# Kernel tuning notes

Hardware: AMD Instinct MI355X
Metric: run time of the kernel (lower is better)

The kernel has to match this reference:

```python
import jax, jax.numpy as jnp
import numpy as np

DISTANCES = [1, 2]
ANGLES_DEG = [0.0, 45.0, 90.0, 135.0]
LEVELS = 32
FEATURES = ["contrast", "homogeneity", "energy", "correlation"]

# skimage graycomatrix offsets: row = r + round(sin(a)*d), col = c + round(cos(a)*d)
OFFSETS = [(int(np.round(np.sin(np.deg2rad(a)) * d)), int(np.round(np.cos(np.deg2rad(a)) * d)))
           for d in DISTANCES for a in ANGLES_DEG]


def _quantize(images, levels):
    # RGB -> gray, [-1,1] -> [0,1] -> integer gray levels (uint8 floor cast in original)
    gray = images.mean(axis=1)                                  # [B,H,W]
    g = jnp.clip((gray + 1.0) * 0.5 * (levels - 1), 0.0, levels - 1)
    return g.astype(jnp.int32)


def _glcm(g, dr, dc, levels):
    # symmetric, normed co-occurrence matrix for one (distance, angle) offset
    B, H, W = g.shape
    r0, r1 = max(0, -dr), H - max(0, dr)
    c0, c1 = max(0, -dc), W - max(0, dc)
    i = g[:, r0:r1, c0:c1]
    j = g[:, r0 + dr:r1 + dr, c0 + dc:c1 + dc]
    idx = (i * levels + j).reshape(B, -1)                        # [B, n_pairs]
    hist = jax.vmap(lambda ix: jnp.zeros(levels * levels, jnp.float32).at[ix].add(1.0))(idx)
    P = hist.reshape(B, levels, levels)
    P = P + jnp.swapaxes(P, 1, 2)                                # symmetric
    return P / jnp.sum(P, axis=(1, 2), keepdims=True)            # normed


def _prop(P, feat):
    # graycoprops formulas; P: [B, L, L]
    L = P.shape[-1]
    I = jnp.arange(L, dtype=jnp.float32)[:, None]                # [L,1]
    J = jnp.arange(L, dtype=jnp.float32)[None, :]                # [1,L]
    if feat == "contrast":
        return jnp.sum(P * (I - J) ** 2, axis=(1, 2))
    if feat == "homogeneity":
        return jnp.sum(P / (1.0 + (I - J) ** 2), axis=(1, 2))
    if feat == "energy":
        return jnp.sqrt(jnp.sum(P * P, axis=(1, 2)))
    if feat == "correlation":
        mu_i = jnp.sum(I * P, axis=(1, 2))                       # [B]
        mu_j = jnp.sum(J * P, axis=(1, 2))
        di = I[None] - mu_i[:, None, None]
        dj = J[None] - mu_j[:, None, None]
        std_i = jnp.sqrt(jnp.sum(P * di * di, axis=(1, 2)))
        std_j = jnp.sqrt(jnp.sum(P * dj * dj, axis=(1, 2)))
        cov = jnp.sum(P * di * dj, axis=(1, 2))
        denom = std_i * std_j
        return jnp.where(denom > 1e-15, cov / jnp.where(denom > 1e-15, denom, 1.0), 1.0)
    raise ValueError(feat)


def reference(images):
    g = _quantize(images, LEVELS)
    # accumulate feature values over all (distance, angle) offsets, then mean
    acc = {f: 0.0 for f in FEATURES}
    for (dr, dc) in OFFSETS:
        P = _glcm(g, dr, dc, LEVELS)
        for f in FEATURES:
            acc[f] = acc[f] + _prop(P, f)
    n = float(len(OFFSETS))
    return jnp.stack([acc[f] / n for f in FEATURES], axis=0)     # [n_features, B]


def setup_inputs() -> dict:
    key = jax.random.key(0)
    images = jax.random.normal(key, (64, 3, 512, 512), dtype=jnp.float32)
    return {"images": images}
```

## Files before the change

kernel.cpp:

```cpp
#include <hip/hip_runtime.h>

#define NIMG 64
#define NUQ 6
#define NSTRIP 16
#define SROWS 32
#define HW (512 * 512)

__device__ __constant__ float UOFF_W[NUQ] = {1.f, 2.f, 1.f, 2.f, 1.f, 1.f};
#define DR_PACK 0x201110u
#define DCP_PACK 0x130122u

__device__ __forceinline__ unsigned char quant1(float x, float y, float z) {
    float gray = (x + y + z) / 3.0f;
    float t = (gray + 1.0f) * 0.5f * 31.0f;
    t = fminf(fmaxf(t, 0.0f), 31.0f);
    return (unsigned char)(int)t;
}

__device__ __forceinline__ void ppair(int i, int j, unsigned int* __restrict__ hu) {
    int d = (i << 4) | ((i + (j >> 1)) & 15);
    atomicAdd(&hu[d], 1u << ((j & 1) << 4));
}

__global__ __launch_bounds__(256) void glcm_fused(
    const float* __restrict__ in, unsigned int* __restrict__ hist_g) {
    const int b = blockIdx.x >> 4;
    const int s = blockIdx.x & 15;
    const int rs = s * SROWS;

    __shared__ unsigned char ring[4 * 2048];
    __shared__ unsigned int hist[NUQ * 512];

    const int tid = threadIdx.x;
    for (int k = tid; k < NUQ * 512; k += 256) hist[k] = 0;

    const float* ib = in + (size_t)b * (3 * HW);
    const int lrow = tid >> 6;
    const int lcol = (tid & 63) << 3;

    float4 A0, B0, A1, B1, A2, B2;

    for (int c = 0; c <= 9; ++c) {
        const int gr = rs + (c << 2) + lrow;
        const bool doload = (c <= 8) && ((c << 2) + lrow < SROWS + 2) && (gr < 512);
        if (doload) {
            const float* p = ib + ((size_t)gr << 9) + lcol;
            A0 = *(const float4*)(p);
            B0 = *(const float4*)(p + 4);
            A1 = *(const float4*)(p + HW);
            B1 = *(const float4*)(p + HW + 4);
            A2 = *(const float4*)(p + 2 * HW);
            B2 = *(const float4*)(p + 2 * HW + 4);
        }

        if (c >= 2) {
            const int k = c - 2;
            for (int idx = tid; idx < 768; idx += 256) {
                int u = idx >> 7;
                int rem = idx & 127;
                int r4 = rem >> 5;
                int g = rem & 31;
                int dr = (DR_PACK >> (u << 2)) & 15;
                int dc = (int)((DCP_PACK >> (u << 2)) & 15) - 1;
                int R = (k << 2) + r4;
                int nr_u = min(512 - dr - rs, SROWS);
                int gA = (dc < 0) ? 1 : 0;
                int gEnd = (dc > 0) ? 31 : 32;
                if (R < nr_u && g >= gA && g < gEnd) {
                    const uint4* ip = (const uint4*)(ring + ((k & 3) << 11) + (r4 << 9) + (g << 4));
                    uint4 iw = *ip;
                    int Rj = R + dr;
                    int jbase = (((Rj >> 2) & 3) << 11) + ((Rj & 3) << 9);
                    unsigned int jw0, jw1, jw2, jw3;
                    if (dc == 0) {
                        uint4 jv = *(const uint4*)(ring + jbase + (g << 4));
                        jw0 = jv.x; jw1 = jv.y; jw2 = jv.z; jw3 = jv.w;
                    } else {
                        int jb = jbase + (g << 4) + dc;
                        const unsigned int* t32 = (const unsigned int*)(ring + (jb & ~3));
                        int sb = (jb & 3) << 3;
                        unsigned int w0 = t32[0], w1 = t32[1], w2 = t32[2],
                                     w3 = t32[3], w4 = t32[4];
                        jw0 = (w0 >> sb) | (w1 << (32 - sb));
                        jw1 = (w1 >> sb) | (w2 << (32 - sb));
                        jw2 = (w2 >> sb) | (w3 << (32 - sb));
                        jw3 = (w3 >> sb) | (w4 << (32 - sb));
                    }
                    unsigned int* hu = hist + (u << 9);
                    #pragma unroll
                    for (int q = 0; q < 4; ++q) {
                        ppair((iw.x >> (8 * q)) & 255, (jw0 >> (8 * q)) & 255, hu);
                        ppair((iw.y >> (8 * q)) & 255, (jw1 >> (8 * q)) & 255, hu);
                        ppair((iw.z >> (8 * q)) & 255, (jw2 >> (8 * q)) & 255, hu);
                        ppair((iw.w >> (8 * q)) & 255, (jw3 >> (8 * q)) & 255, hu);
                    }
                }
            }
            for (int idx = tid; idx < 384; idx += 256) {
                int u = idx >> 6;
                int rem = idx & 63;
                int r4 = rem >> 4;
                int e = rem & 15;
                int dr = (DR_PACK >> (u << 2)) & 15;
                int dc = (int)((DCP_PACK >> (u << 2)) & 15) - 1;
                int elen = (dc == 0) ? 0 : ((dc == 2) ? 14 : 15);
                int ebase = (dc < 0) ? 1 : 496;
                int R = (k << 2) + r4;
                int nr_u = min(512 - dr - rs, SROWS);
                if (e < elen && R < nr_u) {
                    int ci = ebase + e;
                    int ia = ((k & 3) << 11) + (r4 << 9) + ci;
                    int Rj = R + dr;
                    int ja = (((Rj >> 2) & 3) << 11) + ((Rj & 3) << 9) + ci + dc;
                    ppair(ring[ia], ring[ja], hist + (u << 9));
                }
            }
        }

        if (doload) {
            unsigned int q0 =
                (unsigned int)quant1(A0.x, A1.x, A2.x)
                | ((unsigned int)quant1(A0.y, A1.y, A2.y) << 8)
                | ((unsigned int)quant1(A0.z, A1.z, A2.z) << 16)
                | ((unsigned int)quant1(A0.w, A1.w, A2.w) << 24);
            unsigned int q1 =
                (unsigned int)quant1(B0.x, B1.x, B2.x)
                | ((unsigned int)quant1(B0.y, B1.y, B2.y) << 8)
                | ((unsigned int)quant1(B0.z, B1.z, B2.z) << 16)
                | ((unsigned int)quant1(B0.w, B1.w, B2.w) << 24);
            uint2* wp = (uint2*)(ring + ((c & 3) << 11) + (lrow << 9) + lcol);
            *wp = make_uint2(q0, q1);
        }
        __syncthreads();
    }

    unsigned int* hb = hist_g + (size_t)blockIdx.x * (NUQ * 512);
    for (int k = tid; k < NUQ * 512; k += 256) hb[k] = hist[k];
}

__global__ __launch_bounds__(256) void feature_kernel(
    const unsigned int* __restrict__ hist_g, float* __restrict__ feats) {
    const int blk = blockIdx.x;
    const int b = blk / NUQ;
    const int u = blk - b * NUQ;
    const int dr = (DR_PACK >> (u << 2)) & 15;
    const int dc = (int)((DCP_PACK >> (u << 2)) & 15) - 1;
    const int adc = dc < 0 ? -dc : dc;
    const float inv_total = 1.0f / (2.0f * (float)((512 - dr) * (512 - adc)));

    __shared__ unsigned int cnt[1024];
    __shared__ float red[4][6];
    const int tid = threadIdx.x;
    const int wid = tid >> 6;
    const int lane = tid & 63;

    for (int d = tid; d < 512; d += 256) {
        unsigned int lo = 0, hi = 0;
        const unsigned int* p = hist_g + ((size_t)(b * NSTRIP) * NUQ + u) * 512 + d;
        #pragma unroll
        for (int st = 0; st < NSTRIP; ++st) {
            unsigned int v = p[(size_t)st * NUQ * 512];
            lo += v & 0xffffu;
            hi += v >> 16;
        }
        int i = d >> 4;
        int jh = ((d & 15) - i) & 15;
        cnt[(i << 5) | (jh << 1)] = lo;
        cnt[(i << 5) | (jh << 1) | 1] = hi;
    }
    __syncthreads();

    float c_sum = 0.f, h_sum = 0.f, e_sum = 0.f, m1 = 0.f, m2 = 0.f, m12 = 0.f;
    for (int k = tid; k < 1024; k += 256) {
        int i = k >> 5, j = k & 31;
        float sym = (float)(cnt[k] + cnt[(j << 5) | i]);
        float P = sym * inv_total;
        float d = (float)(i - j);
        float d2 = d * d;
        float fi = (float)i, fj = (float)j;
        c_sum += P * d2;
        h_sum += P / (1.0f + d2);
        e_sum += P * P;
        m1  += P * fi;
        m2  += P * fi * fi;
        m12 += P * fi * fj;
    }
    #pragma unroll
    for (int sft = 32; sft > 0; sft >>= 1) {
        c_sum += __shfl_down(c_sum, sft);
        h_sum += __shfl_down(h_sum, sft);
        e_sum += __shfl_down(e_sum, sft);
        m1    += __shfl_down(m1, sft);
        m2    += __shfl_down(m2, sft);
        m12   += __shfl_down(m12, sft);
    }
    if (lane == 0) {
        red[wid][0] = c_sum; red[wid][1] = h_sum; red[wid][2] = e_sum;
        red[wid][3] = m1;    red[wid][4] = m2;    red[wid][5] = m12;
    }
    __syncthreads();
    if (tid == 0) {
        float rc = 0, rh = 0, re2 = 0, rm1 = 0, rm2 = 0, rm12 = 0;
        #pragma unroll
        for (int w = 0; w < 4; ++w) {
            rc += red[w][0]; rh += red[w][1]; re2 += red[w][2];
            rm1 += red[w][3]; rm2 += red[w][4]; rm12 += red[w][5];
        }
        float mu  = rm1;
        float var = rm2 - mu * mu;
        float cov = rm12 - mu * mu;
        float denom = var;
        float corr = (denom > 1e-15f) ? cov / denom : 1.0f;
        float* f = feats + (size_t)blk * 4;
        f[0] = rc;
        f[1] = rh;
        f[2] = sqrtf(re2);
        f[3] = corr;
    }
}

__global__ __launch_bounds__(256) void reduce_kernel(
    const float* __restrict__ feats, float* __restrict__ out) {
    int tid = threadIdx.x;
    int f = tid >> 6, b = tid & 63;
    float s = 0.f;
    #pragma unroll
    for (int u = 0; u < NUQ; ++u) s += UOFF_W[u] * feats[(size_t)(b * NUQ + u) * 4 + f];
    out[f * NIMG + b] = s * 0.125f;
}

extern "C" void kernel_launch(void* const* d_in, const int* in_sizes, int n_in,
                              void* d_out, int out_size, void* d_ws, size_t ws_size,
                              hipStream_t stream) {
    const float* images = (const float*)d_in[0];
    float* out = (float*)d_out;

    unsigned int* hist_g = (unsigned int*)d_ws;
    size_t hbytes = (size_t)NIMG * NSTRIP * NUQ * 512 * sizeof(unsigned int);
    float* feats = (float*)((char*)d_ws + hbytes);

    glcm_fused<<<NIMG * NSTRIP, 256, 0, stream>>>(images, hist_g);
    feature_kernel<<<NIMG * NUQ, 256, 0, stream>>>(hist_g, feats);
    reduce_kernel<<<1, 256, 0, stream>>>(feats, out);
}
```

Measured before the change: 65.28 us.

## Double-buffer global loads in GLCM kernel and fuse feature and reduce kernels

The main histogram kernel now keeps two register sets for loaded tiles, so each tile's global loads are issued one stage before it is quantized. This gives the loads a full histogram stage to complete before their data is used. Separately, the per-offset feature kernel and the final reduce kernel are merged into one kernel per image, which drops a launch and the intermediate feature buffer. The costs are higher register pressure from the duplicated float4 buffers and fewer blocks (64) in the feature stage.

```diff
diff --git a/kernel.cpp b/kernel.cpp
--- a/kernel.cpp
+++ b/kernel.cpp
@@ -38,12 +38,10 @@
     const int lrow = tid >> 6;
     const int lcol = (tid & 63) << 3;
 
-    float4 A0, B0, A1, B1, A2, B2;
-
-    for (int c = 0; c <= 9; ++c) {
+    auto issueL = [&](int c, float4& A0, float4& B0, float4& A1, float4& B1,
+                      float4& A2, float4& B2) {
         const int gr = rs + (c << 2) + lrow;
-        const bool doload = (c <= 8) && ((c << 2) + lrow < SROWS + 2) && (gr < 512);
-        if (doload) {
+        if ((c << 2) + lrow < SROWS + 2 && gr < 512) {
             const float* p = ib + ((size_t)gr << 9) + lcol;
             A0 = *(const float4*)(p);
             B0 = *(const float4*)(p + 4);
@@ -52,72 +50,12 @@
             A2 = *(const float4*)(p + 2 * HW);
             B2 = *(const float4*)(p + 2 * HW + 4);
         }
-
-        if (c >= 2) {
-            const int k = c - 2;
-            for (int idx = tid; idx < 768; idx += 256) {
-                int u = idx >> 7;
-                int rem = idx & 127;
-                int r4 = rem >> 5;
-                int g = rem & 31;
-                int dr = (DR_PACK >> (u << 2)) & 15;
-                int dc = (int)((DCP_PACK >> (u << 2)) & 15) - 1;
-                int R = (k << 2) + r4;
-                int nr_u = min(512 - dr - rs, SROWS);
-                int gA = (dc < 0) ? 1 : 0;
-                int gEnd = (dc > 0) ? 31 : 32;
-                if (R < nr_u && g >= gA && g < gEnd) {
-                    const uint4* ip = (const uint4*)(ring + ((k & 3) << 11) + (r4 << 9) + (g << 4));
-                    uint4 iw = *ip;
-                    int Rj = R + dr;
-                    int jbase = (((Rj >> 2) & 3) << 11) + ((Rj & 3) << 9);
-                    unsigned int jw0, jw1, jw2, jw3;
-                    if (dc == 0) {
-                        uint4 jv = *(const uint4*)(ring + jbase + (g << 4));
-                        jw0 = jv.x; jw1 = jv.y; jw2 = jv.z; jw3 = jv.w;
-                    } else {
-                        int jb = jbase + (g << 4) + dc;
-                        const unsigned int* t32 = (const unsigned int*)(ring + (jb & ~3));
-                        int sb = (jb & 3) << 3;
-                        unsigned int w0 = t32[0], w1 = t32[1], w2 = t32[2],
-                                     w3 = t32[3], w4 = t32[4];
-                        jw0 = (w0 >> sb) | (w1 << (32 - sb));
-                        jw1 = (w1 >> sb) | (w2 << (32 - sb));
-                        jw2 = (w2 >> sb) | (w3 << (32 - sb));
-                        jw3 = (w3 >> sb) | (w4 << (32 - sb));
-                    }
-                    unsigned int* hu = hist + (u << 9);
-                    #pragma unroll
-                    for (int q = 0; q < 4; ++q) {
-                        ppair((iw.x >> (8 * q)) & 255, (jw0 >> (8 * q)) & 255, hu);
-                        ppair((iw.y >> (8 * q)) & 255, (jw1 >> (8 * q)) & 255, hu);
-                        ppair((iw.z >> (8 * q)) & 255, (jw2 >> (8 * q)) & 255, hu);
-                        ppair((iw.w >> (8 * q)) & 255, (jw3 >> (8 * q)) & 255, hu);
-                    }
-                }
-            }
-            for (int idx = tid; idx < 384; idx += 256) {
-                int u = idx >> 6;
-                int rem = idx & 63;
-                int r4 = rem >> 4;
-                int e = rem & 15;
-                int dr = (DR_PACK >> (u << 2)) & 15;
-                int dc = (int)((DCP_PACK >> (u << 2)) & 15) - 1;
-                int elen = (dc == 0) ? 0 : ((dc == 2) ? 14 : 15);
-                int ebase = (dc < 0) ? 1 : 496;
-                int R = (k << 2) + r4;
-                int nr_u = min(512 - dr - rs, SROWS);
-                if (e < elen && R < nr_u) {
-                    int ci = ebase + e;
-                    int ia = ((k & 3) << 11) + (r4 << 9) + ci;
-                    int Rj = R + dr;
-                    int ja = (((Rj >> 2) & 3) << 11) + ((Rj & 3) << 9) + ci + dc;
-                    ppair(ring[ia], ring[ja], hist + (u << 9));
-                }
-            }
-        }
-
-        if (doload) {
+    };
+
+    auto quantW = [&](int c, const float4& A0, const float4& B0, const float4& A1,
+                      const float4& B1, const float4& A2, const float4& B2) {
+        const int gr = rs + (c << 2) + lrow;
+        if ((c << 2) + lrow < SROWS + 2 && gr < 512) {
             unsigned int q0 =
                 (unsigned int)quant1(A0.x, A1.x, A2.x)
                 | ((unsigned int)quant1(A0.y, A1.y, A2.y) << 8)
@@ -131,102 +69,172 @@
             uint2* wp = (uint2*)(ring + ((c & 3) << 11) + (lrow << 9) + lcol);
             *wp = make_uint2(q0, q1);
         }
-        __syncthreads();
+    };
+
+    auto histF = [&](int k) {
+        for (int idx = tid; idx < 768; idx += 256) {
+            int u = idx >> 7;
+            int rem = idx & 127;
+            int r4 = rem >> 5;
+            int g = rem & 31;
+            int dr = (DR_PACK >> (u << 2)) & 15;
+            int dc = (int)((DCP_PACK >> (u << 2)) & 15) - 1;
+            int R = (k << 2) + r4;
+            int nr_u = min(512 - dr - rs, SROWS);
+            int gA = (dc < 0) ? 1 : 0;
+            int gEnd = (dc > 0) ? 31 : 32;
+            if (R < nr_u && g >= gA && g < gEnd) {
+                const uint4* ip = (const uint4*)(ring + ((k & 3) << 11) + (r4 << 9) + (g << 4));
+                uint4 iw = *ip;
+                int Rj = R + dr;
+                int jbase = (((Rj >> 2) & 3) << 11) + ((Rj & 3) << 9);
+                unsigned int jw0, jw1, jw2, jw3;
+                if (dc == 0) {
+                    uint4 jv = *(const uint4*)(ring + jbase + (g << 4));
+                    jw0 = jv.x; jw1 = jv.y; jw2 = jv.z; jw3 = jv.w;
+                } else {
+                    int jb = jbase + (g << 4) + dc;
+                    const unsigned int* t32 = (const unsigned int*)(ring + (jb & ~3));
+                    int sb = (jb & 3) << 3;
+                    unsigned int w0 = t32[0], w1 = t32[1], w2 = t32[2],
+                                 w3 = t32[3], w4 = t32[4];
+                    jw0 = (w0 >> sb) | (w1 << (32 - sb));
+                    jw1 = (w1 >> sb) | (w2 << (32 - sb));
+                    jw2 = (w2 >> sb) | (w3 << (32 - sb));
+                    jw3 = (w3 >> sb) | (w4 << (32 - sb));
+                }
+                unsigned int* hu = hist + (u << 9);
+                #pragma unroll
+                for (int q = 0; q < 4; ++q) {
+                    ppair((iw.x >> (8 * q)) & 255, (jw0 >> (8 * q)) & 255, hu);
+                    ppair((iw.y >> (8 * q)) & 255, (jw1 >> (8 * q)) & 255, hu);
+                    ppair((iw.z >> (8 * q)) & 255, (jw2 >> (8 * q)) & 255, hu);
+                    ppair((iw.w >> (8 * q)) & 255, (jw3 >> (8 * q)) & 255, hu);
+                }
+            }
+        }
+        for (int idx = tid; idx < 384; idx += 256) {
+            int u = idx >> 6;
+            int rem = idx & 63;
+            int r4 = rem >> 4;
+            int e = rem & 15;
+            int dr = (DR_PACK >> (u << 2)) & 15;
+            int dc = (int)((DCP_PACK >> (u << 2)) & 15) - 1;
+            int elen = (dc == 0) ? 0 : ((dc == 2) ? 14 : 15);
+            int ebase = (dc < 0) ? 1 : 496;
+            int R = (k << 2) + r4;
+            int nr_u = min(512 - dr - rs, SROWS);
+            if (e < elen && R < nr_u) {
+                int ci = ebase + e;
+                int ia = ((k & 3) << 11) + (r4 << 9) + ci;
+                int Rj = R + dr;
+                int ja = (((Rj >> 2) & 3) << 11) + ((Rj & 3) << 9) + ci + dc;
+                ppair(ring[ia], ring[ja], hist + (u << 9));
+            }
+        }
+    };
+
+    float4 zA0 = {0,0,0,0}, zB0 = {0,0,0,0}, zA1 = {0,0,0,0},
+           zB1 = {0,0,0,0}, zA2 = {0,0,0,0}, zB2 = {0,0,0,0};
+    float4 yA0 = {0,0,0,0}, yB0 = {0,0,0,0}, yA1 = {0,0,0,0},
+           yB1 = {0,0,0,0}, yA2 = {0,0,0,0}, yB2 = {0,0,0,0};
+
+    for (int cc = 0; cc < 12; cc += 2) {
+        {
+            const int c = cc;
+            if (c <= 8) issueL(c, zA0, zB0, zA1, zB1, zA2, zB2);
+            if (c >= 3 && c <= 10) histF(c - 3);
+            if (c >= 1 && c <= 9) quantW(c - 1, yA0, yB0, yA1, yB1, yA2, yB2);
+            __syncthreads();
+        }
+        {
+            const int c = cc + 1;
+            if (c <= 8) issueL(c, yA0, yB0, yA1, yB1, yA2, yB2);
+            if (c >= 3 && c <= 10) histF(c - 3);
+            if (c >= 1 && c <= 9) quantW(c - 1, zA0, zB0, zA1, zB1, zA2, zB2);
+            __syncthreads();
+        }
     }
 
     unsigned int* hb = hist_g + (size_t)blockIdx.x * (NUQ * 512);
     for (int k = tid; k < NUQ * 512; k += 256) hb[k] = hist[k];
 }
 
-__global__ __launch_bounds__(256) void feature_kernel(
-    const unsigned int* __restrict__ hist_g, float* __restrict__ feats) {
-    const int blk = blockIdx.x;
-    const int b = blk / NUQ;
-    const int u = blk - b * NUQ;
-    const int dr = (DR_PACK >> (u << 2)) & 15;
-    const int dc = (int)((DCP_PACK >> (u << 2)) & 15) - 1;
-    const int adc = dc < 0 ? -dc : dc;
-    const float inv_total = 1.0f / (2.0f * (float)((512 - dr) * (512 - adc)));
-
-    __shared__ unsigned int cnt[1024];
-    __shared__ float red[4][6];
+__global__ __launch_bounds__(256) void feature_out_kernel(
+    const unsigned int* __restrict__ hist_g, float* __restrict__ out) {
+    const int b = blockIdx.x;
+    __shared__ unsigned int cnt[NUQ][1024];
+    __shared__ float fred[NUQ][4];
     const int tid = threadIdx.x;
     const int wid = tid >> 6;
     const int lane = tid & 63;
 
-    for (int d = tid; d < 512; d += 256) {
-        unsigned int lo = 0, hi = 0;
-        const unsigned int* p = hist_g + ((size_t)(b * NSTRIP) * NUQ + u) * 512 + d;
+    for (int u = wid; u < NUQ; u += 4) {
+        const unsigned int* p = hist_g + ((size_t)b * NSTRIP * NUQ + u) * 512;
+        for (int d = lane; d < 512; d += 64) {
+            unsigned int lo = 0, hi = 0;
+            #pragma unroll
+            for (int st = 0; st < NSTRIP; ++st) {
+                unsigned int v = p[(size_t)st * NUQ * 512 + d];
+                lo += v & 0xffffu;
+                hi += v >> 16;
+            }
+            int i = d >> 4;
+            int jh = ((d & 15) - i) & 15;
+            cnt[u][(i << 5) | (jh << 1)] = lo;
+            cnt[u][(i << 5) | (jh << 1) | 1] = hi;
+        }
+    }
+    __syncthreads();
+
+    for (int u = wid; u < NUQ; u += 4) {
+        int dr = (DR_PACK >> (u << 2)) & 15;
+        int dc = (int)((DCP_PACK >> (u << 2)) & 15) - 1;
+        int adc = dc < 0 ? -dc : dc;
+        float inv_total = 1.0f / (2.0f * (float)((512 - dr) * (512 - adc)));
+        float c_sum = 0.f, h_sum = 0.f, e_sum = 0.f, m1 = 0.f, m2 = 0.f, m12 = 0.f;
+        for (int k = lane; k < 1024; k += 64) {
+            int i = k >> 5, j = k & 31;
+            float sym = (float)(cnt[u][k] + cnt[u][(j << 5) | i]);
+            float P = sym * inv_total;
+            float d = (float)(i - j);
+            float d2 = d * d;
+            float fi = (float)i, fj = (float)j;
+            c_sum += P * d2;
+            h_sum += P / (1.0f + d2);
+            e_sum += P * P;
+            m1  += P * fi;
+            m2  += P * fi * fi;
+            m12 += P * fi * fj;
+        }
         #pragma unroll
-        for (int st = 0; st < NSTRIP; ++st) {
-            unsigned int v = p[(size_t)st * NUQ * 512];
-            lo += v & 0xffffu;
-            hi += v >> 16;
-        }
-        int i = d >> 4;
-        int jh = ((d & 15) - i) & 15;
-        cnt[(i << 5) | (jh << 1)] = lo;
-        cnt[(i << 5) | (jh << 1) | 1] = hi;
+        for (int sft = 32; sft > 0; sft >>= 1) {
+            c_sum += __shfl_down(c_sum, sft);
+            h_sum += __shfl_down(h_sum, sft);
+            e_sum += __shfl_down(e_sum, sft);
+            m1    += __shfl_down(m1, sft);
+            m2    += __shfl_down(m2, sft);
+            m12   += __shfl_down(m12, sft);
+        }
+        if (lane == 0) {
+            float mu  = m1;
+            float var = m2 - mu * mu;
+            float cov = m12 - mu * mu;
+            float corr = (var > 1e-15f) ? cov / var : 1.0f;
+            fred[u][0] = c_sum;
+            fred[u][1] = h_sum;
+            fred[u][2] = sqrtf(e_sum);
+            fred[u][3] = corr;
+        }
     }
     __syncthreads();
 
-    float c_sum = 0.f, h_sum = 0.f, e_sum = 0.f, m1 = 0.f, m2 = 0.f, m12 = 0.f;
-    for (int k = tid; k < 1024; k += 256) {
-        int i = k >> 5, j = k & 31;
-        float sym = (float)(cnt[k] + cnt[(j << 5) | i]);
-        float P = sym * inv_total;
-        float d = (float)(i - j);
-        float d2 = d * d;
-        float fi = (float)i, fj = (float)j;
-        c_sum += P * d2;
-        h_sum += P / (1.0f + d2);
-        e_sum += P * P;
-        m1  += P * fi;
-        m2  += P * fi * fi;
-        m12 += P * fi * fj;
-    }
-    #pragma unroll
-    for (int sft = 32; sft > 0; sft >>= 1) {
-        c_sum += __shfl_down(c_sum, sft);
-        h_sum += __shfl_down(h_sum, sft);
-        e_sum += __shfl_down(e_sum, sft);
-        m1    += __shfl_down(m1, sft);
-        m2    += __shfl_down(m2, sft);
-        m12   += __shfl_down(m12, sft);
-    }
-    if (lane == 0) {
-        red[wid][0] = c_sum; red[wid][1] = h_sum; red[wid][2] = e_sum;
-        red[wid][3] = m1;    red[wid][4] = m2;    red[wid][5] = m12;
-    }
-    __syncthreads();
-    if (tid == 0) {
-        float rc = 0, rh = 0, re2 = 0, rm1 = 0, rm2 = 0, rm12 = 0;
+    if (tid < 4) {
+        float s = 0.f;
         #pragma unroll
-        for (int w = 0; w < 4; ++w) {
-            rc += red[w][0]; rh += red[w][1]; re2 += red[w][2];
-            rm1 += red[w][3]; rm2 += red[w][4]; rm12 += red[w][5];
-        }
-        float mu  = rm1;
-        float var = rm2 - mu * mu;
-        float cov = rm12 - mu * mu;
-        float denom = var;
-        float corr = (denom > 1e-15f) ? cov / denom : 1.0f;
-        float* f = feats + (size_t)blk * 4;
-        f[0] = rc;
-        f[1] = rh;
-        f[2] = sqrtf(re2);
-        f[3] = corr;
-    }
-}
-
-__global__ __launch_bounds__(256) void reduce_kernel(
-    const float* __restrict__ feats, float* __restrict__ out) {
-    int tid = threadIdx.x;
-    int f = tid >> 6, b = tid & 63;
-    float s = 0.f;
-    #pragma unroll
-    for (int u = 0; u < NUQ; ++u) s += UOFF_W[u] * feats[(size_t)(b * NUQ + u) * 4 + f];
-    out[f * NIMG + b] = s * 0.125f;
+        for (int u = 0; u < NUQ; ++u) s += UOFF_W[u] * fred[u][tid];
+        out[tid * NIMG + b] = s * 0.125f;
+    }
 }
 
 extern "C" void kernel_launch(void* const* d_in, const int* in_sizes, int n_in,
@@ -236,10 +244,7 @@
     float* out = (float*)d_out;
 
     unsigned int* hist_g = (unsigned int*)d_ws;
-    size_t hbytes = (size_t)NIMG * NSTRIP * NUQ * 512 * sizeof(unsigned int);
-    float* feats = (float*)((char*)d_ws + hbytes);
 
     glcm_fused<<<NIMG * NSTRIP, 256, 0, stream>>>(images, hist_g);
-    feature_kernel<<<NIMG * NUQ, 256, 0, stream>>>(hist_g, feats);
-    reduce_kernel<<<1, 256, 0, stream>>>(feats, out);
-}
+    feature_out_kernel<<<NIMG, 256, 0, stream>>>(hist_g, out);
+}
```

Result: slower. 75.60 us (+15.8%).
